# Optimization experiments

Hardware: AMD Instinct MI355X
Metric: run time of the kernel (lower is better)

The kernel has to match this reference:

```python
import jax, jax.numpy as jnp
import numpy as np

MEM = 256
K = 4
SQRT_MK = 32  # sqrt(MEM*K)
HID = 1024
INP = 1024
B = 8192
EPS = 1e-12


def _linear_params(key, out_f, in_f):
    kw, kb = jax.random.split(key)
    bound = 1.0 / np.sqrt(in_f)
    W = jax.random.uniform(kw, (out_f, in_f), jnp.float32, -bound, bound)
    b = jax.random.uniform(kb, (out_f,), jnp.float32, -bound, bound)
    return W, b


def setup_inputs() -> dict:
    key = jax.random.key(0)
    ks = jax.random.split(key, 8)
    x = jax.random.normal(ks[0], (B, INP), jnp.float32)
    h0 = jax.random.normal(ks[1], (B, HID), jnp.float32)
    memory = jax.random.normal(ks[2], (B, MEM), jnp.float32)
    W_h, b_h = _linear_params(ks[3], HID, MEM + HID + INP)        # hmi2h
    W_a, b_a = _linear_params(ks[4], K, MEM + HID)                # hm2alpha
    W_b, b_b = _linear_params(ks[5], K, MEM + HID)                # hm2beta
    W_va, b_va = _linear_params(ks[6], 2 * SQRT_MK, MEM + HID)    # hm2v_alpha
    W_vb, b_vb = _linear_params(ks[7], 2 * SQRT_MK, MEM + HID)    # hm2v_beta
    return {"x": x, "h0": h0, "memory": memory,
            "W_h": W_h, "b_h": b_h, "W_a": W_a, "b_a": b_a,
            "W_b": W_b, "b_b": b_b, "W_va": W_va, "b_va": b_va,
            "W_vb": W_vb, "b_vb": b_vb}


def _p5_normalize(v):
    # F.normalize(p=5, dim=2): v / max(||v||_5, eps)
    n = jnp.sum(jnp.abs(v) ** 5, axis=2, keepdims=True) ** (1.0 / 5.0)
    return v / jnp.maximum(n, EPS)


def _rank1_v(hm, W, b):
    u = hm @ W.T + b                       # [B, 2*sqrt_mk]
    u0, u1 = u[:, :SQRT_MK], u[:, SQRT_MK:]
    v = (u0[:, :, None] * u1[:, None, :]).reshape(-1, K, MEM)  # outer product
    return _p5_normalize(v)


def reference(x, h0, memory, W_h, b_h, W_a, b_a, W_b, b_b, W_va, b_va, W_vb, b_vb):
    # use_relu=False -> _opt_relu is identity; layer_norm=False -> identity
    c_input = jnp.concatenate([x, h0, memory], axis=1)          # [B, INP+HID+MEM]
    h = jax.nn.relu(c_input @ W_h.T + b_h)                      # [B, HID]
    hm = jnp.concatenate([h, memory], axis=1)                   # [B, HID+MEM]
    alpha = hm @ W_a.T + b_a                                    # [B, K]
    beta = hm @ W_b.T + b_b                                     # [B, K]
    v_alpha = _rank1_v(hm, W_va, b_va)                          # [B, K, MEM]
    v_beta = _rank1_v(hm, W_vb, b_vb)                           # [B, K, MEM]
    delta = alpha[:, :, None] * v_alpha - beta[:, :, None] * v_beta
    memory_new = memory + jnp.mean(delta, axis=1)               # [B, MEM]
    return memory_new, h
```

## Files before the change

### kernel.cpp

```cpp
#include <hip/hip_runtime.h>
#include <stdint.h>

#define B_ROWS 8192
#define INP    1024
#define HID    1024
#define MEMD   256
#define KIN    2304
#define KHM    1280
#define NCAT   144

typedef unsigned short u16;
typedef unsigned int   u32;
typedef __attribute__((ext_vector_type(8))) short bf16x8;
typedef __attribute__((ext_vector_type(4))) float f32x4;

__device__ __forceinline__ u16 f2bf(float f) {
  u32 b = __builtin_bit_cast(u32, f);
  u32 r = b + 0x7FFF + ((b >> 16) & 1);
  return (u16)(r >> 16);
}

__device__ __forceinline__ void gload16(const void* g, void* l) {
  __builtin_amdgcn_global_load_lds(
      (const __attribute__((address_space(1))) u32*)g,
      (__attribute__((address_space(3))) u32*)l, 16, 0, 0);
}

__global__ void k_cvt_xh(const float* __restrict__ x, const float* __restrict__ h0,
                         u16* __restrict__ Abig) {
  const int nIter = B_ROWS * 2048 / 8;
  for (int i = blockIdx.x * blockDim.x + threadIdx.x; i < nIter;
       i += gridDim.x * blockDim.x) {
    int row = i >> 8;
    int col = (i & 255) * 8;
    const float* src = (col < 1024) ? (x + (size_t)row * 1024 + col)
                                    : (h0 + (size_t)row * 1024 + (col - 1024));
    float4 v0 = ((const float4*)src)[0];
    float4 v1 = ((const float4*)src)[1];
    union { u16 u[8]; uint4 q; } pk;
    pk.u[0]=f2bf(v0.x); pk.u[1]=f2bf(v0.y); pk.u[2]=f2bf(v0.z); pk.u[3]=f2bf(v0.w);
    pk.u[4]=f2bf(v1.x); pk.u[5]=f2bf(v1.y); pk.u[6]=f2bf(v1.z); pk.u[7]=f2bf(v1.w);
    *((uint4*)(Abig + (size_t)row * KIN + col)) = pk.q;
  }
}

__global__ void k_cvt_mem(const float* __restrict__ mem,
                          u16* __restrict__ Abig, u16* __restrict__ hm) {
  int i = blockIdx.x * blockDim.x + threadIdx.x;
  int row = i >> 5;
  int col = (i & 31) * 8;
  const float* src = mem + (size_t)row * MEMD + col;
  float4 v0 = ((const float4*)src)[0];
  float4 v1 = ((const float4*)src)[1];
  union { u16 u[8]; uint4 q; } pk;
  pk.u[0]=f2bf(v0.x); pk.u[1]=f2bf(v0.y); pk.u[2]=f2bf(v0.z); pk.u[3]=f2bf(v0.w);
  pk.u[4]=f2bf(v1.x); pk.u[5]=f2bf(v1.y); pk.u[6]=f2bf(v1.z); pk.u[7]=f2bf(v1.w);
  *((uint4*)(Abig + (size_t)row * KIN + 2048 + col)) = pk.q;
  *((uint4*)(hm   + (size_t)row * KHM + 1024 + col)) = pk.q;
}

__global__ void k_cvt_wh(const float* __restrict__ Wh, u16* __restrict__ WhB) {
  int i = blockIdx.x * blockDim.x + threadIdx.x;
  const float* src = Wh + (size_t)i * 8;
  float4 v0 = ((const float4*)src)[0];
  float4 v1 = ((const float4*)src)[1];
  union { u16 u[8]; uint4 q; } pk;
  pk.u[0]=f2bf(v0.x); pk.u[1]=f2bf(v0.y); pk.u[2]=f2bf(v0.z); pk.u[3]=f2bf(v0.w);
  pk.u[4]=f2bf(v1.x); pk.u[5]=f2bf(v1.y); pk.u[6]=f2bf(v1.z); pk.u[7]=f2bf(v1.w);
  *((uint4*)(WhB + (size_t)i * 8)) = pk.q;
}

__global__ void k_cvt_wcat(const float* __restrict__ Wa, const float* __restrict__ ba,
                           const float* __restrict__ Wb, const float* __restrict__ bb,
                           const float* __restrict__ Wva, const float* __restrict__ bva,
                           const float* __restrict__ Wvb, const float* __restrict__ bvb,
                           u16* __restrict__ Wcat, float* __restrict__ bcat) {
  int r = blockIdx.x;
  int t = threadIdx.x;
  const float* src = nullptr; float bias = 0.f;
  if      (r < 4)   { src = Wa  + (size_t)r        * KHM; bias = ba[r];      }
  else if (r < 8)   { src = Wb  + (size_t)(r - 4)  * KHM; bias = bb[r - 4];  }
  else if (r < 72)  { src = Wva + (size_t)(r - 8)  * KHM; bias = bva[r - 8]; }
  else if (r < 136) { src = Wvb + (size_t)(r - 72) * KHM; bias = bvb[r - 72];}
  if (t == 0) bcat[r] = bias;
  if (t < 160) {
    int col = t * 8;
    union { u16 u[8]; uint4 q; } pk;
    if (src) {
      float4 v0 = ((const float4*)(src + col))[0];
      float4 v1 = ((const float4*)(src + col))[1];
      pk.u[0]=f2bf(v0.x); pk.u[1]=f2bf(v0.y); pk.u[2]=f2bf(v0.z); pk.u[3]=f2bf(v0.w);
      pk.u[4]=f2bf(v1.x); pk.u[5]=f2bf(v1.y); pk.u[6]=f2bf(v1.z); pk.u[7]=f2bf(v1.w);
    } else {
      pk.q = make_uint4(0, 0, 0, 0);
    }
    *((uint4*)(Wcat + (size_t)r * KHM + col)) = pk.q;
  }
}

__global__ void k_gemm1(const u16* __restrict__ Abig, const u16* __restrict__ WhB,
                        const float* __restrict__ bh,
                        float* __restrict__ outH, u16* __restrict__ hm) {
  __shared__ u16 As[128 * 64];
  __shared__ u16 Bs[128 * 64];
  const int tid = threadIdx.x;
  const int bid = blockIdx.x;
  const int swz = (bid & 7) * 64 + (bid >> 3);
  const int br = swz >> 3;
  const int bc = swz & 7;
  const int wid = tid >> 6, lane = tid & 63;
  const int wr = wid >> 1, wc = wid & 1;
  const int lr = lane & 15, lko = lane >> 4;

  const f32x4 vz = {0.f, 0.f, 0.f, 0.f};
  f32x4 acc[4][4];
#pragma unroll
  for (int m = 0; m < 4; ++m)
#pragma unroll
    for (int n = 0; n < 4; ++n) acc[m][n] = vz;

  const int sRow = tid >> 3;
  const int sCol = (tid & 7) * 8;
  const u16* gA = Abig + (size_t)(br * 128 + sRow) * KIN + sCol;
  const u16* gB = WhB  + (size_t)(bc * 128 + sRow) * KIN + sCol;

  for (int kt = 0; kt < KIN / 64; ++kt) {
    const int kofs = kt * 64;
#pragma unroll
    for (int q = 0; q < 4; ++q) {
      gload16(gA + (size_t)(q * 32) * KIN + kofs, As + q * 2048 + tid * 8);
      gload16(gB + (size_t)(q * 32) * KIN + kofs, Bs + q * 2048 + tid * 8);
    }
    __syncthreads();
#pragma unroll
    for (int kk = 0; kk < 64; kk += 32) {
      bf16x8 a[4], b[4];
#pragma unroll
      for (int m = 0; m < 4; ++m)
        a[m] = *(const bf16x8*)&As[(wr * 64 + m * 16 + lr) * 64 + kk + lko * 8];
#pragma unroll
      for (int n = 0; n < 4; ++n)
        b[n] = *(const bf16x8*)&Bs[(wc * 64 + n * 16 + lr) * 64 + kk + lko * 8];
#pragma unroll
      for (int m = 0; m < 4; ++m)
#pragma unroll
        for (int n = 0; n < 4; ++n)
          acc[m][n] = __builtin_amdgcn_mfma_f32_16x16x32_bf16(a[m], b[n], acc[m][n], 0, 0, 0);
    }
    __syncthreads();
  }

  const int rowBase = br * 128 + wr * 64;
  const int colBase = bc * 128 + wc * 64;
#pragma unroll
  for (int n = 0; n < 4; ++n) {
    const int col = colBase + n * 16 + lr;
    const float bias = bh[col];
#pragma unroll
    for (int m = 0; m < 4; ++m) {
#pragma unroll
      for (int r = 0; r < 4; ++r) {
        const int row = rowBase + m * 16 + lko * 4 + r;
        float v = fmaxf(acc[m][n][r] + bias, 0.0f);
        outH[(size_t)row * HID + col] = v;
        hm[(size_t)row * KHM + col] = f2bf(v);
      }
    }
  }
}

__device__ __forceinline__ float p5(float x) {
  float a = fabsf(x);
  float a2 = a * a;
  return a2 * a2 * a;
}

__global__ void __launch_bounds__(256, 2)
k_gemm2(const u16* __restrict__ hm, const u16* __restrict__ Wcat,
        const float* __restrict__ bcat,
        const float* __restrict__ mem, float* __restrict__ outM) {
  __shared__ float pS[4][16][148];
  const int tid = threadIdx.x;
  const int bid = blockIdx.x;
  const int wid = tid >> 6, lane = tid & 63;
  const int lr = lane & 15, lko = lane >> 4;
  const int rowBase = bid * 16;

  const f32x4 vz = {0.f, 0.f, 0.f, 0.f};
  f32x4 acc[9];
#pragma unroll
  for (int n = 0; n < 9; ++n) acc[n] = vz;

  const u16* gA = hm   + (size_t)(rowBase + lr) * KHM + lko * 8;
  const u16* gB = Wcat + (size_t)lr * KHM + lko * 8;

  for (int c = 0; c < 5; ++c) {
    const int kofs = (c * 4 + wid) * 64;
#pragma unroll
    for (int h = 0; h < 2; ++h) {
      const int ko = kofs + h * 32;
      bf16x8 a = *(const bf16x8*)(gA + ko);
      bf16x8 b[9];
#pragma unroll
      for (int n = 0; n < 9; ++n)
        b[n] = *(const bf16x8*)(gB + (size_t)(n * 16) * KHM + ko);
#pragma unroll
      for (int n = 0; n < 9; ++n)
        acc[n] = __builtin_amdgcn_mfma_f32_16x16x32_bf16(a, b[n], acc[n], 0, 0, 0);
    }
  }

#pragma unroll
  for (int n = 0; n < 9; ++n)
#pragma unroll
    for (int r = 0; r < 4; ++r)
      pS[wid][lko * 4 + r][n * 16 + lr] = acc[n][r];
  __syncthreads();

  {
    const int rr = tid >> 4;
    const int cb = (tid & 15) * 9;
#pragma unroll
    for (int i = 0; i < 9; ++i) {
      const int col = cb + i;
      float s = pS[0][rr][col] + pS[1][rr][col] + pS[2][rr][col] + pS[3][rr][col]
              + bcat[col];
      pS[0][rr][col] = s;
    }
  }
  __syncthreads();

  const int r = tid >> 4;
  const int t = tid & 15;
  const float* U = &pS[0][r][0];

  float S1a = 0.f, S1b = 0.f;
  {
    const float4* Ua = (const float4*)(U + 40);
    const float4* Ub = (const float4*)(U + 104);
#pragma unroll
    for (int i = 0; i < 8; ++i) {
      float4 va = Ua[i], vb = Ub[i];
      S1a += p5(va.x) + p5(va.y) + p5(va.z) + p5(va.w);
      S1b += p5(vb.x) + p5(vb.y) + p5(vb.z) + p5(vb.w);
    }
  }

  float sa[4], sb[4];
#pragma unroll
  for (int k = 0; k < 4; ++k) {
    const float4* Pa = (const float4*)(U + 8 + 8 * k);
    const float4* Pb = (const float4*)(U + 72 + 8 * k);
    float4 a0v = Pa[0], a1v = Pa[1], b0v = Pb[0], b1v = Pb[1];
    float S0a = p5(a0v.x) + p5(a0v.y) + p5(a0v.z) + p5(a0v.w)
              + p5(a1v.x) + p5(a1v.y) + p5(a1v.z) + p5(a1v.w);
    float S0b = p5(b0v.x) + p5(b0v.y) + p5(b0v.z) + p5(b0v.w)
              + p5(b1v.x) + p5(b1v.y) + p5(b1v.z) + p5(b1v.w);
    float na = exp2f(0.2f * log2f(S0a * S1a));
    float nb = exp2f(0.2f * log2f(S0b * S1b));
    sa[k] = 0.25f * U[k]     / fmaxf(na, 1e-12f);
    sb[k] = 0.25f * U[4 + k] / fmaxf(nb, 1e-12f);
  }

  const int j0 = t >> 1;
  float A0 = 0.f, B0 = 0.f;
#pragma unroll
  for (int k = 0; k < 4; ++k) {
    A0 += sa[k] * U[8  + 8 * k + j0];
    B0 += sb[k] * U[72 + 8 * k + j0];
  }

  const int i1b = (t & 1) * 16;
  const size_t rowg = (size_t)(rowBase + r);
  const float4* memR = (const float4*)(mem  + rowg * MEMD + t * 16);
  float4*       outR = (float4*)      (outM + rowg * MEMD + t * 16);
#pragma unroll
  for (int j = 0; j < 4; ++j) {
    float4 mv = memR[j];
    float4 ua = *(const float4*)(U + 40  + i1b + j * 4);
    float4 ub = *(const float4*)(U + 104 + i1b + j * 4);
    float4 o;
    o.x = mv.x + A0 * ua.x - B0 * ub.x;
    o.y = mv.y + A0 * ua.y - B0 * ub.y;
    o.z = mv.z + A0 * ua.z - B0 * ub.z;
    o.w = mv.w + A0 * ua.w - B0 * ub.w;
    outR[j] = o;
  }
}

extern "C" void kernel_launch(void* const* d_in, const int* in_sizes, int n_in,
                              void* d_out, int out_size, void* d_ws, size_t ws_size,
                              hipStream_t stream) {
  const float* x   = (const float*)d_in[0];
  const float* h0  = (const float*)d_in[1];
  const float* mem = (const float*)d_in[2];
  const float* Wh  = (const float*)d_in[3];
  const float* bh  = (const float*)d_in[4];
  const float* Wa  = (const float*)d_in[5];
  const float* ba  = (const float*)d_in[6];
  const float* Wb  = (const float*)d_in[7];
  const float* bb  = (const float*)d_in[8];
  const float* Wva = (const float*)d_in[9];
  const float* bva = (const float*)d_in[10];
  const float* Wvb = (const float*)d_in[11];
  const float* bvb = (const float*)d_in[12];

  float* outM = (float*)d_out;
  float* outH = (float*)d_out + (size_t)B_ROWS * MEMD;

  char* ws = (char*)d_ws;
  u16*   Abig = (u16*)(ws);
  u16*   WhB  = (u16*)(ws + 37748736);
  u16*   hmB  = (u16*)(ws + 42467328);
  u16*   Wcat = (u16*)(ws + 63438848);
  float* bcat = (float*)(ws + 63807488);

  k_cvt_xh  <<<dim3(2048), dim3(256), 0, stream>>>(x, h0, Abig);
  k_cvt_mem <<<dim3(1024), dim3(256), 0, stream>>>(mem, Abig, hmB);
  k_cvt_wh  <<<dim3(1152), dim3(256), 0, stream>>>(Wh, WhB);
  k_cvt_wcat<<<dim3(144),  dim3(256), 0, stream>>>(Wa, ba, Wb, bb, Wva, bva, Wvb, bvb, Wcat, bcat);
  k_gemm1   <<<dim3(512),  dim3(256), 0, stream>>>(Abig, WhB, bh, outH, hmB);
  k_gemm2   <<<dim3(512),  dim3(256), 0, stream>>>(hmB, Wcat, bcat, mem, outM);
}
```

Baseline: 239.2 us.

## Double-buffer GEMM1 LDS tiles with XOR swizzle and prefetch overlap

The main hidden-layer GEMM now uses two LDS buffers for A and B and prefetches the next K-tile with direct-to-LDS loads while MFMAs run on the current tile, waiting with explicit vmcnt instead of a full sync. LDS columns are XOR-swizzled by row to avoid bank conflicts on the fragment reads, and MFMA sections get raised wave priority. This doubles LDS use to 64KB per block, and launch bounds request 2 blocks per CU, which may limit occupancy or raise register pressure.

After: 226.4 us. 1.06x faster.

```diff
diff --git a/kernel.cpp b/kernel.cpp
--- a/kernel.cpp
+++ b/kernel.cpp
@@ -98,11 +98,12 @@
   }
 }
 
-__global__ void k_gemm1(const u16* __restrict__ Abig, const u16* __restrict__ WhB,
-                        const float* __restrict__ bh,
-                        float* __restrict__ outH, u16* __restrict__ hm) {
-  __shared__ u16 As[128 * 64];
-  __shared__ u16 Bs[128 * 64];
+__global__ void __launch_bounds__(256, 2)
+k_gemm1(const u16* __restrict__ Abig, const u16* __restrict__ WhB,
+        const float* __restrict__ bh,
+        float* __restrict__ outH, u16* __restrict__ hm) {
+  __shared__ u16 As[2][128 * 64];
+  __shared__ u16 Bs[2][128 * 64];
   const int tid = threadIdx.x;
   const int bid = blockIdx.x;
   const int swz = (bid & 7) * 64 + (bid >> 3);
@@ -119,35 +120,71 @@
 #pragma unroll
     for (int n = 0; n < 4; ++n) acc[m][n] = vz;
 
-  const int sRow = tid >> 3;
-  const int sCol = (tid & 7) * 8;
-  const u16* gA = Abig + (size_t)(br * 128 + sRow) * KIN + sCol;
-  const u16* gB = WhB  + (size_t)(bc * 128 + sRow) * KIN + sCol;
+  const int sRow   = tid >> 3;
+  const int sSlotG = (tid & 7) ^ (sRow & 7);
+  const u16* gA = Abig + (size_t)(br * 128 + sRow) * KIN + sSlotG * 8;
+  const u16* gB = WhB  + (size_t)(bc * 128 + sRow) * KIN + sSlotG * 8;
+
+  const int sx  = lr & 7;
+  const int s0  = ((0 + lko) ^ sx) * 8;
+  const int s1  = ((4 + lko) ^ sx) * 8;
+  const int axr = (wr * 64 + lr) * 64;
+  const int bxr = (wc * 64 + lr) * 64;
+
+#pragma unroll
+  for (int q = 0; q < 4; ++q) {
+    gload16(gA + (size_t)(q * 32) * KIN, &As[0][q * 2048 + tid * 8]);
+    gload16(gB + (size_t)(q * 32) * KIN, &Bs[0][q * 2048 + tid * 8]);
+  }
 
   for (int kt = 0; kt < KIN / 64; ++kt) {
-    const int kofs = kt * 64;
-#pragma unroll
-    for (int q = 0; q < 4; ++q) {
-      gload16(gA + (size_t)(q * 32) * KIN + kofs, As + q * 2048 + tid * 8);
-      gload16(gB + (size_t)(q * 32) * KIN + kofs, Bs + q * 2048 + tid * 8);
-    }
-    __syncthreads();
-#pragma unroll
-    for (int kk = 0; kk < 64; kk += 32) {
+    const int cur = kt & 1;
+    if (kt < KIN / 64 - 1) {
+      const int kofs = (kt + 1) * 64;
+#pragma unroll
+      for (int q = 0; q < 4; ++q) {
+        gload16(gA + (size_t)(q * 32) * KIN + kofs, &As[1 - cur][q * 2048 + tid * 8]);
+        gload16(gB + (size_t)(q * 32) * KIN + kofs, &Bs[1 - cur][q * 2048 + tid * 8]);
+      }
+      asm volatile("s_waitcnt vmcnt(8)" ::: "memory");
+    } else {
+      asm volatile("s_waitcnt vmcnt(0)" ::: "memory");
+    }
+    __builtin_amdgcn_s_barrier();
+    __builtin_amdgcn_sched_barrier(0);
+
+    const u16* Ac = &As[cur][0];
+    const u16* Bc = &Bs[cur][0];
+    {
       bf16x8 a[4], b[4];
 #pragma unroll
-      for (int m = 0; m < 4; ++m)
-        a[m] = *(const bf16x8*)&As[(wr * 64 + m * 16 + lr) * 64 + kk + lko * 8];
-#pragma unroll
-      for (int n = 0; n < 4; ++n)
-        b[n] = *(const bf16x8*)&Bs[(wc * 64 + n * 16 + lr) * 64 + kk + lko * 8];
+      for (int m = 0; m < 4; ++m) a[m] = *(const bf16x8*)&Ac[axr + m * 1024 + s0];
+#pragma unroll
+      for (int n = 0; n < 4; ++n) b[n] = *(const bf16x8*)&Bc[bxr + n * 1024 + s0];
+      __builtin_amdgcn_s_setprio(1);
 #pragma unroll
       for (int m = 0; m < 4; ++m)
 #pragma unroll
         for (int n = 0; n < 4; ++n)
           acc[m][n] = __builtin_amdgcn_mfma_f32_16x16x32_bf16(a[m], b[n], acc[m][n], 0, 0, 0);
-    }
-    __syncthreads();
+      __builtin_amdgcn_s_setprio(0);
+    }
+    {
+      bf16x8 a[4], b[4];
+#pragma unroll
+      for (int m = 0; m < 4; ++m) a[m] = *(const bf16x8*)&Ac[axr + m * 1024 + s1];
+#pragma unroll
+      for (int n = 0; n < 4; ++n) b[n] = *(const bf16x8*)&Bc[bxr + n * 1024 + s1];
+      __builtin_amdgcn_s_setprio(1);
+#pragma unroll
+      for (int m = 0; m < 4; ++m)
+#pragma unroll
+        for (int n = 0; n < 4; ++n)
+          acc[m][n] = __builtin_amdgcn_mfma_f32_16x16x32_bf16(a[m], b[n], acc[m][n], 0, 0, 0);
+      __builtin_amdgcn_s_setprio(0);
+    }
+    __builtin_amdgcn_sched_barrier(0);
+    __builtin_amdgcn_s_barrier();
   }
 
   const int rowBase = br * 128 + wr * 64;
```
